# Optimization experiments

Hardware: AMD Instinct MI355X
Metric: run time of the kernel (lower is better)

## Reference

```python
import jax, jax.numpy as jnp
import numpy as np

N_NODES = 100000
N_EDGES = 3200000
IN_DIM = 128
HID_DIM = 128


def setup_inputs() -> dict:
    key = jax.random.key(0)
    k1, k2, k3, k4, k5 = jax.random.split(key, 5)
    h = jax.random.normal(k1, (N_NODES, IN_DIM), dtype=jnp.float32)
    src = jax.random.randint(k2, (N_EDGES,), 0, N_NODES, dtype=jnp.int64)
    dst = jax.random.randint(k3, (N_EDGES,), 0, N_NODES, dtype=jnp.int64)
    # TAGConv k=1 linear: in_features = 2*IN_DIM, out = HID_DIM
    W = jax.random.normal(k4, (2 * IN_DIM, HID_DIM), dtype=jnp.float32) * (1.0 / np.sqrt(2 * IN_DIM))
    b = jax.random.normal(k5, (HID_DIM,), dtype=jnp.float32) * 0.01
    return {"h": h, "src": src, "dst": dst, "W": W, "b": b}


def reference(h, src, dst, W, b):
    N = h.shape[0]
    # symmetric normalization D^{-1/2} A D^{-1/2} using in-degrees (DGL TAGConv)
    deg = jax.ops.segment_sum(jnp.ones_like(dst, dtype=h.dtype), dst, num_segments=N)
    norm = jnp.clip(deg, 1.0, None) ** -0.5  # [N]
    hn = h * norm[:, None]
    # gather from src, scatter-add into dst  (A @ hn)
    agg = jax.ops.segment_sum(hn[src], dst, num_segments=N)
    agg = agg * norm[:, None]
    # TAGConv k=1: concat powers [h, A_norm h] -> linear
    fstack = jnp.concatenate([h, agg], axis=-1)  # [N, 2*IN_DIM]
    out = fstack @ W + b  # [N, HID]
    # Normalize(power=2): x / (sum x^2)^(1/2), no eps
    nrm = jnp.sqrt(jnp.sum(out * out, axis=1, keepdims=True))
    return out / nrm
```

## Files before the change

### kernel.cpp

```cpp
#include <hip/hip_runtime.h>
#include <hip/hip_fp16.h>

#define N_NODES 100000
#define IN_DIM 128
#define HID_DIM 128
#define GM 64
#define NB 196
#define BCAP 17200
#define TILE 4096
#define NR 4

typedef __attribute__((ext_vector_type(8))) short bf16x8;
typedef __attribute__((ext_vector_type(4))) float f32x4;
typedef __attribute__((ext_vector_type(2))) float f32x2;

#if defined(__has_builtin)
#if __has_builtin(__builtin_amdgcn_cvt_pk_f32_fp8) && __has_builtin(__builtin_amdgcn_cvt_pk_fp8_f32)
#define HAVE_FP8CVT 1
#endif
#endif
#ifndef HAVE_FP8CVT
#define HAVE_FP8CVT 0
#endif

#if HAVE_FP8CVT
#define DEC_SCALE (1.0f / 16.0f)
#else
#define DEC_SCALE (256.0f / 16.0f)
#endif

__device__ inline ushort bf16rne(float x) {
    uint u = __float_as_uint(x);
    return (ushort)((u + 0x7FFFu + ((u >> 16) & 1u)) >> 16);
}

__device__ inline uint enc4_fp8(float a, float b, float c, float d) {
#if HAVE_FP8CVT
    int r = 0;
    r = __builtin_amdgcn_cvt_pk_fp8_f32(a, b, r, false);
    r = __builtin_amdgcn_cvt_pk_fp8_f32(c, d, r, true);
    return (uint)r;
#else
    float vv[4] = {a, b, c, d};
    uint out = 0;
#pragma unroll
    for (int i = 0; i < 4; i++) {
        __half hh = __float2half(vv[i] * (1.0f / 256.0f));
        ushort hb = *reinterpret_cast<ushort*>(&hh);
        uint s = ((uint)hb >> 8) & 0x80u;
        uint em = ((uint)hb >> 7) & 0x7Fu;
        em += ((uint)hb >> 6) & 1u;
        if (em > 0x7Eu) em = 0x7Eu;
        out |= (s | em) << (8 * i);
    }
    return out;
#endif
}

__device__ inline void dec4_acc2(uint u, f32x2* acc) {
#if HAVE_FP8CVT
    f32x2 a0 = __builtin_amdgcn_cvt_pk_f32_fp8((int)u, false);
    f32x2 a1 = __builtin_amdgcn_cvt_pk_f32_fp8((int)u, true);
    acc[0] += a0;
    acc[1] += a1;
#else
    float f[4];
#pragma unroll
    for (int i = 0; i < 4; i++) {
        uint byte = (u >> (8 * i)) & 0xFFu;
        ushort hb = (ushort)(((byte & 0x80u) << 8) | ((byte & 0x7Fu) << 7));
        __half hh = *reinterpret_cast<__half*>(&hb);
        f[i] = __half2float(hh);
    }
    acc[0] += (f32x2){f[0], f[1]};
    acc[1] += (f32x2){f[2], f[3]};
#endif
}

__global__ __launch_bounds__(256) void p1_bin_kernel(
    const int* __restrict__ src, const int* __restrict__ dst,
    int* __restrict__ bcursor, uint* __restrict__ binned, int nE) {
    __shared__ uint staged[TILE];
    __shared__ uchar bid[TILE];
    __shared__ int cnt[256];
    __shared__ int scn[256];
    __shared__ int cur[256];
    __shared__ int gbase[256];
    int t = threadIdx.x;
    int e0 = blockIdx.x * TILE;
    int tilecnt = nE - e0; if (tilecnt > TILE) tilecnt = TILE;

    cnt[t] = 0;
    __syncthreads();

    int es[16], ed[16];
    int vk[4];
#pragma unroll
    for (int k = 0; k < 4; k++) {
        int base = e0 + (k * 256 + t) * 4;
        vk[k] = (base < nE);
        if (vk[k]) {
            int4 s4 = *(const int4*)(src + base);
            int4 d4 = *(const int4*)(dst + base);
            es[k*4+0]=s4.x; es[k*4+1]=s4.y; es[k*4+2]=s4.z; es[k*4+3]=s4.w;
            ed[k*4+0]=d4.x; ed[k*4+1]=d4.y; ed[k*4+2]=d4.z; ed[k*4+3]=d4.w;
        }
    }
#pragma unroll
    for (int k = 0; k < 4; k++)
        if (vk[k]) {
#pragma unroll
            for (int j = 0; j < 4; j++) atomicAdd(&cnt[ed[k*4+j] >> 9], 1);
        }
    __syncthreads();
    scn[t] = cnt[t];
    __syncthreads();
    for (int d = 1; d < 256; d <<= 1) {
        int v = (t >= d) ? scn[t - d] : 0;
        __syncthreads();
        scn[t] += v;
        __syncthreads();
    }
    int excl = scn[t] - cnt[t];
    __syncthreads();
    scn[t] = excl;
    cur[t] = excl;
    if (t < NB) gbase[t] = atomicAdd(&bcursor[t], cnt[t]);
    __syncthreads();
#pragma unroll
    for (int k = 0; k < 4; k++)
        if (vk[k]) {
#pragma unroll
            for (int j = 0; j < 4; j++) {
                int d = ed[k*4+j];
                int b = d >> 9;
                int r = atomicAdd(&cur[b], 1);
                staged[r] = (uint)es[k*4+j] | ((uint)(d & 511) << 17);
                bid[r] = (uchar)b;
            }
        }
    __syncthreads();
    for (int i = t; i < tilecnt; i += 256) {
        uint p = staged[i];
        int b = bid[i];
        int off = gbase[b] + (i - scn[b]);
        if (off < BCAP) binned[(long)b * BCAP + off] = p;
    }
}

__global__ __launch_bounds__(1024) void p2_fill_kernel(
    const uint* __restrict__ binned, const int* __restrict__ bcursor,
    int* __restrict__ lists, int* __restrict__ off_g, int* __restrict__ degi,
    float* __restrict__ norm, uint* __restrict__ off_rg, int N) {
    __shared__ int cnt2[512 * NR];
    __shared__ int off2[512 * NR];
    __shared__ int temp[1024];
    __shared__ int stage[BCAP];
    int b = blockIdx.x;
    int t = threadIdx.x;
    int cnt = bcursor[b]; if (cnt > BCAP) cnt = BCAP;
    const uint* eb = binned + (long)b * BCAP;
    int d0 = b << 9;

    for (int k = t; k < 512 * NR; k += 1024) cnt2[k] = 0;
    __syncthreads();
    for (int i = t; i < cnt; i += 1024) {
        uint p = eb[i];
        int key = (int)(p >> 17) * NR + (int)((p & 0x1FFFFu) >> 15);
        atomicAdd(&cnt2[key], 1);
    }
    __syncthreads();
    int b2 = t * 2;
    int l0 = cnt2[b2], l1 = cnt2[b2 + 1];
    temp[t] = l0 + l1;
    __syncthreads();
    for (int d = 1; d < 1024; d <<= 1) {
        int v = (t >= d) ? temp[t - d] : 0;
        __syncthreads();
        temp[t] += v;
        __syncthreads();
    }
    int tb = (t == 0) ? 0 : temp[t - 1];
    off2[b2] = tb;
    off2[b2 + 1] = tb + l0;
    __syncthreads();
    if (t < 512) {
        int node = d0 + t;
        if (node < N) {
            int S = off2[t * NR];
            int nxt = (t < 511) ? off2[t * NR + NR] : cnt;
            int dg = nxt - S;
            degi[node] = dg;
            off_g[node] = b * BCAP + S;
            norm[node] = rsqrtf((float)(dg < 1 ? 1 : dg));
            uint rg = 0;
            rg |= (uint)(off2[t * NR + 1] - S) & 0xFFu;
            rg |= ((uint)(off2[t * NR + 2] - S) & 0xFFu) << 8;
            rg |= ((uint)(off2[t * NR + 3] - S) & 0xFFu) << 16;
            off_rg[node] = rg;
        }
    }
    for (int k = t; k < 512 * NR; k += 1024) cnt2[k] = 0;
    __syncthreads();
    for (int i = t; i < cnt; i += 1024) {
        uint p = eb[i];
        int sv = (int)(p & 0x1FFFFu);
        int key = (int)(p >> 17) * NR + (sv >> 15);
        int pos = off2[key] + atomicAdd(&cnt2[key], 1);
        stage[pos] = sv;
    }
    __syncthreads();
    for (int i = t; i < cnt; i += 1024) lists[(long)b * BCAP + i] = stage[i];
}

__global__ void prep_kernel(const float* __restrict__ h, const float* __restrict__ norm,
                            uint* __restrict__ hn8, ushort* __restrict__ hbf, int N) {
    int t = blockIdx.x * blockDim.x + threadIdx.x;
    int node = t >> 4;
    if (node > N) return;
    uint2 o = make_uint2(0, 0);
    if (node < N) {
        int c = (t & 15) * 8;
        float nm = norm[node] * 16.0f;
        const float* p = h + (long)node * IN_DIM + c;
        float4 a = ((const float4*)p)[0];
        float4 bb = ((const float4*)p)[1];
        o.x = enc4_fp8(a.x * nm, a.y * nm, a.z * nm, a.w * nm);
        o.y = enc4_fp8(bb.x * nm, bb.y * nm, bb.z * nm, bb.w * nm);
        uint4 hb;
        hb.x = (uint)bf16rne(a.x)  | ((uint)bf16rne(a.y) << 16);
        hb.y = (uint)bf16rne(a.z)  | ((uint)bf16rne(a.w) << 16);
        hb.z = (uint)bf16rne(bb.x) | ((uint)bf16rne(bb.y) << 16);
        hb.w = (uint)bf16rne(bb.z) | ((uint)bf16rne(bb.w) << 16);
        *(uint4*)(hbf + (long)node * IN_DIM + c) = hb;
    }
    ((uint2*)hn8)[t] = o;
}

__global__ void wconv_kernel(const float* __restrict__ W, ushort* __restrict__ wt) {
    int t = blockIdx.x * blockDim.x + threadIdx.x;
    int j = t >> 8, k = t & 255;
    wt[t] = bf16rne(W[k * HID_DIM + j]);
}

__global__ __launch_bounds__(512) void fused_kernel(
    const ushort* __restrict__ hbf, const uint* __restrict__ hn8,
    const int* __restrict__ lists, const int* __restrict__ off_g,
    const int* __restrict__ degi, const float* __restrict__ norm,
    const uint* __restrict__ off_rg, const ushort* __restrict__ wt,
    const float* __restrict__ bias, float* __restrict__ out, int N) {
    int t = threadIdx.x;
    int w = t >> 6;
    int l = t & 63;
    int n0 = blockIdx.x * GM;

    __shared__ __align__(16) ushort rows[GM][264];
    __shared__ float partial[8][GM];

    for (int f = t; f < GM * 16; f += 512) {
        int m = f >> 4, c = (f & 15) * 8;
        int n = n0 + m;
        uint4 v = make_uint4(0, 0, 0, 0);
        if (n < N) v = *(const uint4*)(hbf + (long)n * IN_DIM + c);
        *(uint4*)&rows[m][c] = v;
    }

    {
        int g = l >> 3, sub = l & 7;
        int m = w * 8 + g;
        int node = n0 + m;
        bool valid = node < N;
        int deg = valid ? degi[node] : 0;
        int S = valid ? off_g[node] : 0;
        uint rsw = valid ? off_rg[node] : 0;
        f32x2 acc2[8];
#pragma unroll
        for (int q = 0; q < 8; q++) acc2[q] = (f32x2){0.0f, 0.0f};
        const char* rowbase = (const char*)hn8;
        uint c16 = (uint)sub * 16u;
        int st = 0;
#pragma unroll
        for (int r = 0; r < NR; r++) {
            int en = (r < 3) ? (int)((rsw >> (8 * r)) & 0xFFu) : deg;
            int len = en - st;
            int mx = len;
            mx = max(mx, __shfl_xor(mx, 8));
            mx = max(mx, __shfl_xor(mx, 16));
            mx = max(mx, __shfl_xor(mx, 32));
            for (int base = 0; base < mx; base += 8) {
                int myidx = (sub < len - base) ? lists[S + st + base + sub] : 0;
                int kmax = mx - base; if (kmax > 8) kmax = 8;
                for (int k = 0; k < kmax; k++) {
                    int s2 = __shfl(myidx, (g << 3) | k);
                    if (base + k >= len) s2 = N;
                    uint4 v = *(const uint4*)(rowbase + ((((uint)s2) << 7) | c16));
                    dec4_acc2(v.x, acc2 + 0);
                    dec4_acc2(v.y, acc2 + 2);
                    dec4_acc2(v.z, acc2 + 4);
                    dec4_acc2(v.w, acc2 + 6);
                }
            }
            st = en;
        }
        float nm = valid ? norm[node] * DEC_SCALE : 0.0f;
        uint rr[8];
#pragma unroll
        for (int q = 0; q < 8; q++) {
            uint lo = (uint)bf16rne(acc2[q].x * nm);
            uint hi = (uint)bf16rne(acc2[q].y * nm);
            rr[q] = lo | (hi << 16);
        }
        *(uint4*)&rows[m][IN_DIM + c16] = make_uint4(rr[0], rr[1], rr[2], rr[3]);
        *(uint4*)&rows[m][IN_DIM + c16 + 8] = make_uint4(rr[4], rr[5], rr[6], rr[7]);
    }

    bf16x8 bfrag[8];
    {
        int colA = 16 * w + (l & 15);
        int ko = (l >> 4) * 8;
#pragma unroll
        for (int kt = 0; kt < 8; kt++)
            bfrag[kt] = *(const bf16x8*)(wt + (long)colA * 256 + kt * 32 + ko);
    }

    float bj = bias[16 * w + (l & 15)];
    f32x4 cacc[4];
#pragma unroll
    for (int mt = 0; mt < 4; mt++) cacc[mt] = (f32x4){bj, bj, bj, bj};
    __syncthreads();

#pragma unroll
    for (int kt = 0; kt < 8; kt++) {
        int kbyte = kt * 64 + (l >> 4) * 16;
#pragma unroll
        for (int mt = 0; mt < 4; mt++) {
            int row = mt * 16 + (l & 15);
            bf16x8 a = *(const bf16x8*)((const char*)&rows[row][0] + kbyte);
            cacc[mt] = __builtin_amdgcn_mfma_f32_16x16x32_bf16(a, bfrag[kt], cacc[mt], 0, 0, 0);
        }
    }

#pragma unroll
    for (int mt = 0; mt < 4; mt++)
#pragma unroll
        for (int i = 0; i < 4; i++) {
            float s = cacc[mt][i] * cacc[mt][i];
            s += __shfl_xor(s, 1);
            s += __shfl_xor(s, 2);
            s += __shfl_xor(s, 4);
            s += __shfl_xor(s, 8);
            if ((l & 15) == 0) partial[w][mt * 16 + (l >> 4) * 4 + i] = s;
        }
    __syncthreads();

#pragma unroll
    for (int mt = 0; mt < 4; mt++)
#pragma unroll
        for (int i = 0; i < 4; i++) {
            int r = mt * 16 + (l >> 4) * 4 + i;
            int n = n0 + r;
            if (n < N) {
                float ssum = partial[0][r] + partial[1][r] + partial[2][r] + partial[3][r]
                           + partial[4][r] + partial[5][r] + partial[6][r] + partial[7][r];
                float inv = rsqrtf(ssum);
                out[(long)n * HID_DIM + 16 * w + (l & 15)] = cacc[mt][i] * inv;
            }
        }
}

extern "C" void kernel_launch(void* const* d_in, const int* in_sizes, int n_in,
                              void* d_out, int out_size, void* d_ws, size_t ws_size,
                              hipStream_t stream) {
    const float* h   = (const float*)d_in[0];
    const int*   src = (const int*)d_in[1];
    const int*   dst = (const int*)d_in[2];
    const float* W   = (const float*)d_in[3];
    const float* b   = (const float*)d_in[4];
    float* out = (float*)d_out;

    const int N  = N_NODES;
    const int nE = in_sizes[1];

    char* ws = (char*)d_ws;
    int*  lists   = (int*)ws;       ws += (size_t)NB * BCAP * 4;
    int*  off_g   = (int*)ws;       ws += (size_t)N * 4;
    int*  degi    = (int*)ws;       ws += (size_t)N * 4;
    float* norm   = (float*)ws;     ws += (size_t)N * 4;
    int*  bcursor = (int*)ws;       ws += (size_t)(NB + 4) * 4;
    ushort* wt    = (ushort*)ws;    ws += (size_t)HID_DIM * 2 * IN_DIM * 2;
    uint* off_rg  = (uint*)ws;      ws += (size_t)N * 4;
    ushort* hbf   = (ushort*)ws;    ws += (size_t)N * IN_DIM * 2;
    char* uni     = ws;
    uint* binned  = (uint*)uni;
    uint* hn8     = (uint*)uni;

    hipMemsetAsync(bcursor, 0, (size_t)NB * 4, stream);

    wconv_kernel<<<(2 * IN_DIM * HID_DIM) / 256, 256, 0, stream>>>(W, wt);

    int p1_blocks = (nE + TILE - 1) / TILE;
    p1_bin_kernel<<<p1_blocks, 256, 0, stream>>>(src, dst, bcursor, binned, nE);
    p2_fill_kernel<<<NB, 1024, 0, stream>>>(binned, bcursor, lists, off_g, degi, norm, off_rg, N);

    int prep_units = (N + 1) * 16;
    prep_kernel<<<(prep_units + 255) / 256, 256, 0, stream>>>(h, norm, hn8, hbf, N);

    fused_kernel<<<(N + GM - 1) / GM, 512, 0, stream>>>(
        hbf, hn8, lists, off_g, degi, norm, off_rg, wt, b, out, N);
}
```

Measured before the change: 178.7 us.

## Split neighbor lists into 8 source-range buckets, fold memset into wconv

```diff
diff --git a/kernel.cpp b/kernel.cpp
--- a/kernel.cpp
+++ b/kernel.cpp
@@ -8,7 +8,7 @@
 #define NB 196
 #define BCAP 17200
 #define TILE 4096
-#define NR 4
+#define NR 8
 
 typedef __attribute__((ext_vector_type(8))) short bf16x8;
 typedef __attribute__((ext_vector_type(4))) float f32x4;
@@ -151,7 +151,7 @@
 __global__ __launch_bounds__(1024) void p2_fill_kernel(
     const uint* __restrict__ binned, const int* __restrict__ bcursor,
     int* __restrict__ lists, int* __restrict__ off_g, int* __restrict__ degi,
-    float* __restrict__ norm, uint* __restrict__ off_rg, int N) {
+    float* __restrict__ norm, uint2* __restrict__ off_rg, int N) {
     __shared__ int cnt2[512 * NR];
     __shared__ int off2[512 * NR];
     __shared__ int temp[1024];
@@ -166,13 +166,13 @@
     __syncthreads();
     for (int i = t; i < cnt; i += 1024) {
         uint p = eb[i];
-        int key = (int)(p >> 17) * NR + (int)((p & 0x1FFFFu) >> 15);
+        int key = (int)(p >> 17) * NR + (int)((p & 0x1FFFFu) >> 14);
         atomicAdd(&cnt2[key], 1);
     }
     __syncthreads();
-    int b2 = t * 2;
-    int l0 = cnt2[b2], l1 = cnt2[b2 + 1];
-    temp[t] = l0 + l1;
+    int b4 = t * 4;
+    int l0 = cnt2[b4], l1 = cnt2[b4 + 1], l2 = cnt2[b4 + 2], l3 = cnt2[b4 + 3];
+    temp[t] = l0 + l1 + l2 + l3;
     __syncthreads();
     for (int d = 1; d < 1024; d <<= 1) {
         int v = (t >= d) ? temp[t - d] : 0;
@@ -181,8 +181,10 @@
         __syncthreads();
     }
     int tb = (t == 0) ? 0 : temp[t - 1];
-    off2[b2] = tb;
-    off2[b2 + 1] = tb + l0;
+    off2[b4] = tb;
+    off2[b4 + 1] = tb + l0;
+    off2[b4 + 2] = tb + l0 + l1;
+    off2[b4 + 3] = tb + l0 + l1 + l2;
     __syncthreads();
     if (t < 512) {
         int node = d0 + t;
@@ -193,11 +195,12 @@
             degi[node] = dg;
             off_g[node] = b * BCAP + S;
             norm[node] = rsqrtf((float)(dg < 1 ? 1 : dg));
-            uint rg = 0;
-            rg |= (uint)(off2[t * NR + 1] - S) & 0xFFu;
-            rg |= ((uint)(off2[t * NR + 2] - S) & 0xFFu) << 8;
-            rg |= ((uint)(off2[t * NR + 3] - S) & 0xFFu) << 16;
-            off_rg[node] = rg;
+            uint lo = 0, hi = 0;
+#pragma unroll
+            for (int r = 0; r < 4; r++) lo |= ((uint)(off2[t * NR + r] - S) & 0xFFu) << (8 * r);
+#pragma unroll
+            for (int r = 4; r < 8; r++) hi |= ((uint)(off2[t * NR + r] - S) & 0xFFu) << (8 * (r - 4));
+            off_rg[node] = make_uint2(lo, hi);
         }
     }
     for (int k = t; k < 512 * NR; k += 1024) cnt2[k] = 0;
@@ -205,7 +208,7 @@
     for (int i = t; i < cnt; i += 1024) {
         uint p = eb[i];
         int sv = (int)(p & 0x1FFFFu);
-        int key = (int)(p >> 17) * NR + (sv >> 15);
+        int key = (int)(p >> 17) * NR + (sv >> 14);
         int pos = off2[key] + atomicAdd(&cnt2[key], 1);
         stage[pos] = sv;
     }
@@ -237,8 +240,10 @@
     ((uint2*)hn8)[t] = o;
 }
 
-__global__ void wconv_kernel(const float* __restrict__ W, ushort* __restrict__ wt) {
+__global__ void wconv_kernel(const float* __restrict__ W, ushort* __restrict__ wt,
+                             int* __restrict__ bcursor) {
     int t = blockIdx.x * blockDim.x + threadIdx.x;
+    if (blockIdx.x == 0 && threadIdx.x < NB + 4) bcursor[threadIdx.x] = 0;
     int j = t >> 8, k = t & 255;
     wt[t] = bf16rne(W[k * HID_DIM + j]);
 }
@@ -247,7 +252,7 @@
     const ushort* __restrict__ hbf, const uint* __restrict__ hn8,
     const int* __restrict__ lists, const int* __restrict__ off_g,
     const int* __restrict__ degi, const float* __restrict__ norm,
-    const uint* __restrict__ off_rg, const ushort* __restrict__ wt,
+    const uint2* __restrict__ off_rg, const ushort* __restrict__ wt,
     const float* __restrict__ bias, float* __restrict__ out, int N) {
     int t = threadIdx.x;
     int w = t >> 6;
@@ -272,7 +277,7 @@
         bool valid = node < N;
         int deg = valid ? degi[node] : 0;
         int S = valid ? off_g[node] : 0;
-        uint rsw = valid ? off_rg[node] : 0;
+        uint2 rsw = valid ? off_rg[node] : make_uint2(0, 0);
         f32x2 acc2[8];
 #pragma unroll
         for (int q = 0; q < 8; q++) acc2[q] = (f32x2){0.0f, 0.0f};
@@ -281,7 +286,9 @@
         int st = 0;
 #pragma unroll
         for (int r = 0; r < NR; r++) {
-            int en = (r < 3) ? (int)((rsw >> (8 * r)) & 0xFFu) : deg;
+            int en = (r < 7)
+                ? (int)((r + 1 < 4 ? (rsw.x >> (8 * (r + 1))) : (rsw.y >> (8 * (r - 3)))) & 0xFFu)
+                : deg;
             int len = en - st;
             int mx = len;
             mx = max(mx, __shfl_xor(mx, 8));
@@ -289,8 +296,8 @@
             mx = max(mx, __shfl_xor(mx, 32));
             for (int base = 0; base < mx; base += 8) {
                 int myidx = (sub < len - base) ? lists[S + st + base + sub] : 0;
-                int kmax = mx - base; if (kmax > 8) kmax = 8;
-                for (int k = 0; k < kmax; k++) {
+#pragma unroll
+                for (int k = 0; k < 8; k++) {
                     int s2 = __shfl(myidx, (g << 3) | k);
                     if (base + k >= len) s2 = N;
                     uint4 v = *(const uint4*)(rowbase + ((((uint)s2) << 7) | c16));
@@ -388,15 +395,13 @@
     float* norm   = (float*)ws;     ws += (size_t)N * 4;
     int*  bcursor = (int*)ws;       ws += (size_t)(NB + 4) * 4;
     ushort* wt    = (ushort*)ws;    ws += (size_t)HID_DIM * 2 * IN_DIM * 2;
-    uint* off_rg  = (uint*)ws;      ws += (size_t)N * 4;
+    uint2* off_rg = (uint2*)ws;     ws += (size_t)N * 8;
     ushort* hbf   = (ushort*)ws;    ws += (size_t)N * IN_DIM * 2;
     char* uni     = ws;
     uint* binned  = (uint*)uni;
     uint* hn8     = (uint*)uni;
 
-    hipMemsetAsync(bcursor, 0, (size_t)NB * 4, stream);
-
-    wconv_kernel<<<(2 * IN_DIM * HID_DIM) / 256, 256, 0, stream>>>(W, wt);
+    wconv_kernel<<<(2 * IN_DIM * HID_DIM) / 256, 256, 0, stream>>>(W, wt, bcursor);
 
     int p1_blocks = (nE + TILE - 1) / TILE;
     p1_bin_kernel<<<p1_blocks, 256, 0, stream>>>(src, dst, bcursor, binned, nE);
```

New measurement: 217.6 us. 21.8% more time.
